# Kernel optimization log

Measured on AMD Instinct MI355X. Metric: run time of the kernel, lower is better.

The kernel has to match this reference:

```python
import jax, jax.numpy as jnp
import numpy as np

N_SITE, N_VENDOR, E = 100000, 20000, 3200000
SITE_IN, VENDOR_IN, HID, OUT = 10, 9, 64, 32


def _sage(x_src, x_dst, src, dst, n_dst, Wl, bl, Wr):
    # PyG SAGEConv (mean aggr): lin_l(mean_{e: dst(e)=i} x_src[src(e)]) + lin_r(x_dst)
    msg = x_src[src]                                   # [E, d] gather
    agg = jax.ops.segment_sum(msg, dst, num_segments=n_dst)
    cnt = jax.ops.segment_sum(jnp.ones((src.shape[0],), x_src.dtype), dst,
                              num_segments=n_dst)
    mean = agg / jnp.maximum(cnt, 1.0)[:, None]
    return mean @ Wl + bl + x_dst @ Wr


def setup_inputs() -> dict:
    key = jax.random.key(0)
    ks = jax.random.split(key, 24)
    g = lambda k, s: (jax.random.normal(k, s, jnp.float32) / np.sqrt(s[0])).astype(jnp.float32)
    inp = {
        'x_site': jax.random.normal(ks[0], (N_SITE, SITE_IN), jnp.float32),
        'x_vendor': jax.random.normal(ks[1], (N_VENDOR, VENDOR_IN), jnp.float32),
        'src': jax.random.randint(ks[2], (E,), 0, N_SITE),
        'dst': jax.random.randint(ks[3], (E,), 0, N_VENDOR),
        # input projections
        'W_site_in': g(ks[4], (SITE_IN, HID)), 'b_site_in': jnp.zeros((HID,), jnp.float32),
        'W_vendor_in': g(ks[5], (VENDOR_IN, HID)), 'b_vendor_in': jnp.zeros((HID,), jnp.float32),
        # conv1 site->vendor (64->64)
        'Wl1sv': g(ks[6], (HID, HID)), 'bl1sv': jnp.zeros((HID,), jnp.float32), 'Wr1sv': g(ks[7], (HID, HID)),
        # conv1 vendor->site (64->64)
        'Wl1vs': g(ks[8], (HID, HID)), 'bl1vs': jnp.zeros((HID,), jnp.float32), 'Wr1vs': g(ks[9], (HID, HID)),
        # conv2 site->vendor (64->32)
        'Wl2sv': g(ks[10], (HID, OUT)), 'bl2sv': jnp.zeros((OUT,), jnp.float32), 'Wr2sv': g(ks[11], (HID, OUT)),
        # conv2 vendor->site (64->32)
        'Wl2vs': g(ks[12], (HID, OUT)), 'bl2vs': jnp.zeros((OUT,), jnp.float32), 'Wr2vs': g(ks[13], (HID, OUT)),
    }
    return inp


def reference(x_site, x_vendor, src, dst,
              W_site_in, b_site_in, W_vendor_in, b_vendor_in,
              Wl1sv, bl1sv, Wr1sv, Wl1vs, bl1vs, Wr1vs,
              Wl2sv, bl2sv, Wr2sv, Wl2vs, bl2vs, Wr2vs):
    xs = x_site @ W_site_in + b_site_in        # [N_SITE, HID]
    xv = x_vendor @ W_vendor_in + b_vendor_in  # [N_VENDOR, HID]
    # layer 1 (dropout is identity in eval mode)
    xv1 = jax.nn.relu(_sage(xs, xv, src, dst, N_VENDOR, Wl1sv, bl1sv, Wr1sv))
    xs1 = jax.nn.relu(_sage(xv, xs, dst, src, N_SITE, Wl1vs, bl1vs, Wr1vs))
    # layer 2
    xv2 = jax.nn.relu(_sage(xs1, xv1, src, dst, N_VENDOR, Wl2sv, bl2sv, Wr2sv))
    xs2 = jax.nn.relu(_sage(xv1, xs1, dst, src, N_SITE, Wl2vs, bl2vs, Wr2vs))
    # concat [site; vendor] -> [N_SITE + N_VENDOR, OUT]
    return jnp.concatenate([xs2, xv2], axis=0)
```

## Files before the change

kernel.cpp:

```cpp
#include <hip/hip_runtime.h>

constexpr int N_SITE    = 100000;
constexpr int N_VENDOR  = 20000;
constexpr int NE        = 3200000;
constexpr int SITE_IN   = 10;
constexpr int VENDOR_IN = 9;
constexpr int HID       = 64;
constexpr int OUT       = 32;
constexpr int S_HALF    = 50000;

constexpr int NBLK    = 512;
constexpr int EPB     = NE / NBLK;
constexpr int SHIFT_S = 7;
constexpr int NBUK_S  = (N_SITE + 127) / 128;
constexpr int CAP_S   = 5120;
constexpr int SHIFT_V = 6;
constexpr int NBUK_V  = (N_VENDOR + 63) / 64;
constexpr int CAP_V   = 12288;

constexpr int SB1  = (N_SITE + 3) / 4;
constexpr int VB1  = (N_VENDOR + 3) / 4;
constexpr int NS_BLK = (N_SITE + 15) / 16;
constexpr int NV_BLK = (N_VENDOR + 15) / 16;
constexpr int PADTOT = 16 * (N_SITE + N_VENDOR);

constexpr long long I_NSTART_S = 0;
constexpr long long I_NDEG_S   = I_NSTART_S + N_SITE;
constexpr long long I_NSTART_V = I_NDEG_S + N_SITE;
constexpr long long I_NDEG_V   = I_NSTART_V + N_VENDOR;
constexpr long long I_NLO_V    = I_NDEG_V + N_VENDOR;
constexpr long long I_GCUR     = I_NLO_V + N_VENDOR;
constexpr long long I_ADJ_V    = (I_GCUR + NBUK_S + NBUK_V + 3) & ~3LL;
constexpr long long I_ADJ_S    = I_ADJ_V + (long long)NBUK_V * CAP_V;
constexpr long long INT_END    = (I_ADJ_S + (long long)NBUK_S * CAP_S / 2 + 3) & ~3LL;
constexpr long long A_PAIRS_S  = INT_END;
constexpr long long A_PAIRS_V  = A_PAIRS_S + (long long)NBUK_S * CAP_S;
constexpr long long BUILD_END  = A_PAIRS_V + (long long)NBUK_V * CAP_V;
constexpr long long F_Y16    = (BUILD_END + 3) & ~3LL;
constexpr long long F_PAD    = F_Y16 + (long long)(N_SITE + N_VENDOR) * 16;
constexpr long long F_FUSED  = F_PAD + (long long)(N_SITE + N_VENDOR) * 8;
constexpr long long WS_WORDS = F_FUSED + 4352;

constexpr int F_M1SV = 0;
constexpr int F_M1VS = 1024;
constexpr int F_R1SV = 2048;
constexpr int F_R1VS = 3072;
constexpr int F_V1SV = 4096;
constexpr int F_V1VS = 4160;
constexpr int F_r1SV = 4224;
constexpr int F_r1VS = 4288;

typedef _Float16 h2_t __attribute__((ext_vector_type(2)));
__device__ __forceinline__ h2_t as_h2(unsigned u) {
    union { unsigned u; h2_t h; } c; c.u = u; return c.h;
}
__device__ __forceinline__ unsigned short f2h(float f) {
    union { _Float16 h; unsigned short u; } c; c.h = (_Float16)f; return c.u;
}
#if defined(__has_builtin)
#if __has_builtin(__builtin_amdgcn_fdot2)
#define HAVE_FDOT2 1
#endif
#endif
__device__ __forceinline__ void acc2(float& slo, float& shi, unsigned u) {
#ifdef HAVE_FDOT2
    h2_t sel_lo = {(_Float16)1.0f, (_Float16)0.0f};
    h2_t sel_hi = {(_Float16)0.0f, (_Float16)1.0f};
    slo = __builtin_amdgcn_fdot2(as_h2(u), sel_lo, slo, false);
    shi = __builtin_amdgcn_fdot2(as_h2(u), sel_hi, shi, false);
#else
    h2_t h = as_h2(u);
    slo += (float)h.x; shi += (float)h.y;
#endif
}
__device__ __forceinline__ float ddot2(unsigned a, unsigned b, float c) {
#ifdef HAVE_FDOT2
    return __builtin_amdgcn_fdot2(as_h2(a), as_h2(b), c, false);
#else
    h2_t ha = as_h2(a), hb = as_h2(b);
    return c + (float)ha.x * (float)hb.x + (float)ha.y * (float)hb.y;
#endif
}

__global__ __launch_bounds__(256) void prep(
        const float* __restrict__ x_site, const float* __restrict__ x_vendor,
        unsigned short* __restrict__ xsp, unsigned short* __restrict__ xvp,
        const float* __restrict__ Wsi, const float* __restrict__ bsi,
        const float* __restrict__ Wvi, const float* __restrict__ bvi,
        const float* __restrict__ Wl1sv, const float* __restrict__ Wr1sv,
        const float* __restrict__ Wl1vs, const float* __restrict__ Wr1vs,
        float* __restrict__ fused) {
    long long t = (long long)blockIdx.x * 256 + threadIdx.x;
    if (t < (long long)N_SITE * 16) {
        int i = (int)(t >> 4), k = (int)(t & 15);
        xsp[t] = f2h(k < SITE_IN ? x_site[i * SITE_IN + k] : 0.f);
        return;
    }
    t -= (long long)N_SITE * 16;
    if (t < (long long)N_VENDOR * 16) {
        int i = (int)(t >> 4), k = (int)(t & 15);
        xvp[t] = f2h(k < VENDOR_IN ? x_vendor[i * VENDOR_IN + k] : 0.f);
        return;
    }
    t -= (long long)N_VENDOR * 16;
    int idx = (int)t;
    if (idx < 4096) {
        int m = idx >> 10, rem = idx & 1023, r = rem >> 6, c = rem & 63;
        int K = (m == 0 || m == 3) ? SITE_IN : VENDOR_IN;
        const float* A = (m == 0 || m == 3) ? Wsi : Wvi;
        const float* B = (m == 0) ? Wl1sv : (m == 1) ? Wl1vs : (m == 2) ? Wr1sv : Wr1vs;
        float s = 0.f;
        if (r < K)
            for (int j = 0; j < 64; ++j) s = fmaf(A[r * 64 + j], B[j * 64 + c], s);
        fused[idx] = s;
    } else if (idx < 4352) {
        int m = (idx - 4096) >> 6, c = idx & 63;
        const float* a = (m == 0 || m == 3) ? bsi : bvi;
        const float* B = (m == 0) ? Wl1sv : (m == 1) ? Wl1vs : (m == 2) ? Wr1sv : Wr1vs;
        float s = 0.f;
        for (int j = 0; j < 64; ++j) s = fmaf(a[j], B[j * 64 + c], s);
        fused[idx] = s;
    }
}

__global__ __launch_bounds__(256) void scatter_sort(
        const int* __restrict__ src, const int* __restrict__ dst,
        int* __restrict__ gcur,
        unsigned* __restrict__ pairs_s, unsigned* __restrict__ pairs_v) {
    __shared__ unsigned buf[EPB];
    __shared__ unsigned short bkt[EPB];
    __shared__ int hcnt[NBUK_S];
    __shared__ int loff[NBUK_S + 1];
    __shared__ int gbase[NBUK_S];
    __shared__ int sc[256];
    int blk = blockIdx.x, tid = threadIdx.x;
    int lo = blk * EPB;
    #pragma unroll 1
    for (int dir = 0; dir < 2; ++dir) {
        const int nbuk  = dir ? NBUK_V : NBUK_S;
        const int shift = dir ? SHIFT_V : SHIFT_S;
        const int* key  = dir ? dst : src;
        const int* val  = dir ? src : dst;
        const int goff  = dir ? NBUK_S : 0;
        const long long cap = dir ? CAP_V : CAP_S;
        unsigned* pairs = dir ? pairs_v : pairs_s;
        for (int i = tid; i < nbuk; i += 256) hcnt[i] = 0;
        __syncthreads();
        for (int e = lo + tid; e < lo + EPB; e += 256)
            atomicAdd(&hcnt[key[e] >> shift], 1);
        __syncthreads();
        int base_i = tid * 4;
        int c4[4], s = 0;
        #pragma unroll
        for (int k = 0; k < 4; ++k) {
            int i = base_i + k;
            int c = (i < nbuk) ? hcnt[i] : 0;
            c4[k] = s; s += c;
        }
        sc[tid] = s; __syncthreads();
        for (int st = 1; st < 256; st <<= 1) {
            int x = (tid >= st) ? sc[tid - st] : 0; __syncthreads();
            sc[tid] += x; __syncthreads();
        }
        int pre = tid ? sc[tid - 1] : 0;
        #pragma unroll
        for (int k = 0; k < 4; ++k) {
            int i = base_i + k;
            if (i < nbuk) loff[i] = pre + c4[k];
        }
        if (tid == 0) loff[nbuk] = EPB;
        __syncthreads();
        for (int i = tid; i < nbuk; i += 256) {
            int c = hcnt[i];
            gbase[i] = c ? atomicAdd(&gcur[goff + i], c) : 0;
        }
        __syncthreads();
        for (int i = tid; i < nbuk; i += 256) hcnt[i] = loff[i];
        __syncthreads();
        for (int e = lo + tid; e < lo + EPB; e += 256) {
            int kk = key[e], vv = val[e];
            int b = kk >> shift;
            int p = atomicAdd(&hcnt[b], 1);
            buf[p] = dir ? (((unsigned)(kk & 63) << 26) | (unsigned)vv)
                         : (((unsigned)(kk & 127) << 25) | (unsigned)vv);
            bkt[p] = (unsigned short)b;
        }
        __syncthreads();
        for (int t = tid; t < EPB; t += 256) {
            int b = bkt[t];
            int rel = gbase[b] + (t - loff[b]);
            if (rel < (int)cap)
                pairs[(long long)b * cap + rel] = buf[t];
        }
        __syncthreads();
    }
}

__global__ __launch_bounds__(256) void stage2both(
        const unsigned* __restrict__ pairs_s, const unsigned* __restrict__ pairs_v,
        const int* __restrict__ gcur,
        int* __restrict__ nstart_s, int* __restrict__ ndeg_s,
        int* __restrict__ nstart_v, int* __restrict__ ndeg_v,
        int* __restrict__ nlo_v,
        unsigned short* __restrict__ adj_s16, int* __restrict__ adj_v) {
    int b = blockIdx.x, tid = threadIdx.x;
    bool site = (b < NBUK_S);
    __shared__ int deg[128];
    __shared__ int cur[128];
    __shared__ int sc[256];
    if (site) {
        int lo_node = b << SHIFT_S;
        long long p0 = (long long)b * CAP_S;
        int cnt = min(gcur[b], CAP_S);
        long long p1 = p0 + cnt;
        if (tid < 128) deg[tid] = 0;
        __syncthreads();
        for (long long e = p0 + tid; e < p1; e += 256)
            atomicAdd(&deg[(int)(pairs_s[e] >> 25)], 1);
        __syncthreads();
        int d = (tid < 128) ? deg[tid] : 0;
        sc[tid] = d;
        __syncthreads();
        for (int st = 1; st < 256; st <<= 1) {
            int x = (tid >= st) ? sc[tid - st] : 0; __syncthreads();
            sc[tid] += x; __syncthreads();
        }
        int excl = sc[tid] - d;
        if (tid < 128) {
            int node = lo_node + tid;
            if (node < N_SITE) {
                nstart_s[node] = (int)(p0 + excl);
                ndeg_s[node] = d;
            }
            cur[tid] = (int)(p0 + excl);
        }
        __syncthreads();
        for (long long e = p0 + tid; e < p1; e += 256) {
            unsigned p = pairs_s[e];
            int pos = atomicAdd(&cur[(int)(p >> 25)], 1);
            adj_s16[pos] = (unsigned short)p;
        }
    } else {
        b -= NBUK_S;
        int lo_node = b << SHIFT_V;
        long long p0 = (long long)b * CAP_V;
        int cnt = min(gcur[NBUK_S + b], CAP_V);
        long long p1 = p0 + cnt;
        if (tid < 128) deg[tid] = 0;
        __syncthreads();
        for (long long e = p0 + tid; e < p1; e += 256) {
            unsigned p = pairs_v[e];
            int l = (int)(p >> 26);
            int st = (int)(p & 0x3FFFFFFu);
            atomicAdd(&deg[l], 1);
            if (st < S_HALF) atomicAdd(&deg[64 + l], 1);
        }
        __syncthreads();
        int d = (tid < 64) ? deg[tid] : 0;
        sc[tid] = d;
        __syncthreads();
        for (int st = 1; st < 256; st <<= 1) {
            int x = (tid >= st) ? sc[tid - st] : 0; __syncthreads();
            sc[tid] += x; __syncthreads();
        }
        int excl = sc[tid] - d;
        if (tid < 64) {
            int node = lo_node + tid;
            int dlo = deg[64 + tid];
            if (node < N_VENDOR) {
                nstart_v[node] = (int)(p0 + excl);
                ndeg_v[node] = d;
                nlo_v[node] = dlo;
            }
            cur[tid] = (int)(p0 + excl);
            cur[64 + tid] = (int)(p0 + excl) + dlo;
        }
        __syncthreads();
        for (long long e = p0 + tid; e < p1; e += 256) {
            unsigned p = pairs_v[e];
            int l = (int)(p >> 26);
            int st = (int)(p & 0x3FFFFFFu);
            int pos = atomicAdd((st < S_HALF) ? &cur[l] : &cur[64 + l], 1);
            adj_v[pos] = st;
        }
    }
}

template<typename IdxT>
__device__ __forceinline__ void gather1x(const unsigned short* __restrict__ fp,
                                         const IdxT* __restrict__ adj,
                                         int lo, int hi, int l16, float* s) {
    for (int j = lo + l16; j < hi; j += 16) {
        const unsigned short* row = fp + (long long)adj[j] * 16;
        uint4 q0 = *(const uint4*)row;
        unsigned u4 = *(const unsigned*)(row + 8);
        acc2(s[0], s[1], q0.x);
        acc2(s[2], s[3], q0.y);
        acc2(s[4], s[5], q0.z);
        acc2(s[6], s[7], q0.w);
        acc2(s[8], s[9], u4);
    }
}

__global__ __launch_bounds__(256) void gc1fused(
        const unsigned short* __restrict__ xsp, const unsigned short* __restrict__ xvp,
        const float* __restrict__ xs_raw, const float* __restrict__ xv_raw,
        const int* __restrict__ nstart_s, const int* __restrict__ ndeg_s,
        const unsigned short* __restrict__ adj_s16,
        const int* __restrict__ nstart_v, const int* __restrict__ ndeg_v,
        const int* __restrict__ adj_v,
        const float* __restrict__ fused,
        const float* __restrict__ bl1vs, const float* __restrict__ bl1sv,
        const float* __restrict__ Wl2sv, const float* __restrict__ Wr2vs,
        const float* __restrict__ Wl2vs, const float* __restrict__ Wr2sv,
        unsigned short* __restrict__ ys16, unsigned short* __restrict__ yv16,
        float* __restrict__ out) {
    __shared__ unsigned sWp[32 * 64];
    __shared__ unsigned sXp[16][34];
    int b = blockIdx.x, tid = threadIdx.x;
    bool site = (b < NS_BLK);
    const float *fsraw, *M, *V, *BL, *R, *RV, *Wl, *Wr;
    const int *nst, *ndg;
    unsigned short* Y; float* Z;
    int nodebase, n, kx;
    if (site) {
        nodebase = b * 16; n = N_SITE; kx = SITE_IN;
        fsraw = xs_raw; nst = nstart_s; ndg = ndeg_s;
        M = fused + F_M1VS; V = fused + F_V1VS; BL = bl1vs;
        R = fused + F_R1VS; RV = fused + F_r1VS;
        Wl = Wl2sv; Wr = Wr2vs; Y = ys16; Z = out;
    } else {
        nodebase = (b - NS_BLK) * 16; n = N_VENDOR; kx = VENDOR_IN;
        fsraw = xv_raw; nst = nstart_v; ndg = ndeg_v;
        M = fused + F_M1SV; V = fused + F_V1SV; BL = bl1sv;
        R = fused + F_R1SV; RV = fused + F_r1SV;
        Wl = Wl2vs; Wr = Wr2sv; Y = yv16;
        Z = out + (long long)N_SITE * OUT;
    }
    for (int i = tid; i < 2048; i += 256) {
        int kk = i >> 6, c = i & 63;
        int k0 = kk * 2, k1 = k0 + 1;
        float w0 = (c < 32) ? Wl[k0 * 32 + c] : Wr[k0 * 32 + (c - 32)];
        float w1 = (c < 32) ? Wl[k1 * 32 + c] : Wr[k1 * 32 + (c - 32)];
        sWp[i] = (unsigned)f2h(w0) | ((unsigned)f2h(w1) << 16);
    }
    int l16 = tid & 15, nib = tid >> 4;
    int w = nodebase + nib;
    int c0 = l16 * 4;
    if (w < n) {
        int lo = nst[w], deg = ndg[w], hi = lo + deg;
        float s[10];
        #pragma unroll
        for (int k = 0; k < 10; ++k) s[k] = 0.f;
        if (site) gather1x(xvp, adj_s16, lo, hi, l16, s);
        else      gather1x(xsp, adj_v,   lo, hi, l16, s);
        #pragma unroll
        for (int k = 0; k < 10; ++k) {
            s[k] += __shfl_xor(s[k], 1, 64);
            s[k] += __shfl_xor(s[k], 2, 64);
            s[k] += __shfl_xor(s[k], 4, 64);
            s[k] += __shfl_xor(s[k], 8, 64);
        }
        float inv = 1.0f / (float)max(deg, 1);
        float4 acc = *(const float4*)(BL + c0);
        float4 rv4 = *(const float4*)(RV + c0);
        acc.x += rv4.x; acc.y += rv4.y; acc.z += rv4.z; acc.w += rv4.w;
        if (deg > 0) {
            float4 v4 = *(const float4*)(V + c0);
            acc.x += v4.x; acc.y += v4.y; acc.z += v4.z; acc.w += v4.w;
        }
        #pragma unroll
        for (int k = 0; k < 10; ++k) {
            float m = s[k] * inv;
            float4 m4 = *(const float4*)(M + k * 64 + c0);
            acc.x = fmaf(m, m4.x, acc.x);
            acc.y = fmaf(m, m4.y, acc.y);
            acc.z = fmaf(m, m4.z, acc.z);
            acc.w = fmaf(m, m4.w, acc.w);
        }
        const float* xr = fsraw + (long long)w * kx;
        for (int k = 0; k < kx; ++k) {
            float xv = xr[k];
            float4 r4 = *(const float4*)(R + k * 64 + c0);
            acc.x = fmaf(xv, r4.x, acc.x);
            acc.y = fmaf(xv, r4.y, acc.y);
            acc.z = fmaf(xv, r4.z, acc.z);
            acc.w = fmaf(xv, r4.w, acc.w);
        }
        unsigned plo = (unsigned)f2h(fmaxf(acc.x, 0.f)) |
                       ((unsigned)f2h(fmaxf(acc.y, 0.f)) << 16);
        unsigned phi = (unsigned)f2h(fmaxf(acc.z, 0.f)) |
                       ((unsigned)f2h(fmaxf(acc.w, 0.f)) << 16);
        *(uint2*)&sXp[nib][l16 * 2] = make_uint2(plo, phi);
    }
    __syncthreads();
    int n2 = tid >> 4, q = tid & 15;
    int node = nodebase + n2;
    float4 acc = {0.f, 0.f, 0.f, 0.f};
    const unsigned* xrow = sXp[n2];
    #pragma unroll 8
    for (int kk = 0; kk < 32; ++kk) {
        unsigned xp = xrow[kk];
        uint4 wp = *(const uint4*)(sWp + kk * 64 + q * 4);
        acc.x = ddot2(xp, wp.x, acc.x);
        acc.y = ddot2(xp, wp.y, acc.y);
        acc.z = ddot2(xp, wp.z, acc.z);
        acc.w = ddot2(xp, wp.w, acc.w);
    }
    if (node < n) {
        if (q < 8) {
            unsigned p01 = (unsigned)f2h(acc.x) | ((unsigned)f2h(acc.y) << 16);
            unsigned p23 = (unsigned)f2h(acc.z) | ((unsigned)f2h(acc.w) << 16);
            *(uint2*)(Y + (long long)node * 32 + q * 4) = make_uint2(p01, p23);
        } else {
            *(float4*)(Z + (long long)node * 32 + (q - 8) * 4) = acc;
        }
    }
}

template<typename IdxT>
__device__ __forceinline__ void gather2(const unsigned short* __restrict__ y,
                                        const IdxT* __restrict__ adj,
                                        int lo, int deg, int g, int q,
                                        float& s0, float& s1, float& s2, float& s3) {
    int m = (deg > g) ? ((deg - g + 7) >> 3) : 0;
    const IdxT* ap = adj + lo + g;
    int t = 0;
    for (; t + 4 <= m; t += 4) {
        long long a0 = (long long)ap[8 * t];
        long long a1 = (long long)ap[8 * t + 8];
        long long a2 = (long long)ap[8 * t + 16];
        long long a3 = (long long)ap[8 * t + 24];
        uint2 u0 = *(const uint2*)(y + a0 * 32 + 4 * q);
        uint2 u1 = *(const uint2*)(y + a1 * 32 + 4 * q);
        uint2 u2 = *(const uint2*)(y + a2 * 32 + 4 * q);
        uint2 u3 = *(const uint2*)(y + a3 * 32 + 4 * q);
        acc2(s0, s1, u0.x); acc2(s2, s3, u0.y);
        acc2(s0, s1, u1.x); acc2(s2, s3, u1.y);
        acc2(s0, s1, u2.x); acc2(s2, s3, u2.y);
        acc2(s0, s1, u3.x); acc2(s2, s3, u3.y);
    }
    for (; t < m; ++t) {
        long long a0 = (long long)ap[8 * t];
        uint2 u0 = *(const uint2*)(y + a0 * 32 + 4 * q);
        acc2(s0, s1, u0.x); acc2(s2, s3, u0.y);
    }
}

__global__ __launch_bounds__(256) void gc2all(
        const unsigned short* __restrict__ ys16, const unsigned short* __restrict__ yv16,
        const int* __restrict__ nstart_s, const int* __restrict__ ndeg_s,
        const unsigned short* __restrict__ adj_s16,
        const int* __restrict__ nstart_v, const int* __restrict__ ndeg_v,
        const int* __restrict__ nlo_v,
        const int* __restrict__ adj_v,
        const float* __restrict__ bl2vs, const float* __restrict__ bl2sv,
        float* __restrict__ out) {
    int b = blockIdx.x;
    bool site = (b < SB1);
    const float* bias; float* o; int w, n;
    if (site) {
        w = b * 4 + (threadIdx.x >> 6); n = N_SITE;
        bias = bl2vs; o = out;
    } else {
        w = (b - SB1) * 4 + (threadIdx.x >> 6); n = N_VENDOR;
        bias = bl2sv;
        o = out + (long long)N_SITE * OUT;
    }
    if (w >= n) return;
    int lane = threadIdx.x & 63, g = lane >> 3, q = lane & 7;
    float s0 = 0.f, s1 = 0.f, s2 = 0.f, s3 = 0.f;
    int deg;
    if (site) {
        int lo = nstart_s[w]; deg = ndeg_s[w];
        gather2(yv16, adj_s16, lo, deg, g, q, s0, s1, s2, s3);
    } else {
        int lo = nstart_v[w]; deg = ndeg_v[w];
        int nlo = nlo_v[w];
        gather2(ys16, adj_v, lo, nlo, g, q, s0, s1, s2, s3);
        gather2(ys16, adj_v, lo + nlo, deg - nlo, g, q, s0, s1, s2, s3);
    }
    #pragma unroll
    for (int m = 8; m <= 32; m <<= 1) {
        s0 += __shfl_xor(s0, m, 64);
        s1 += __shfl_xor(s1, m, 64);
        s2 += __shfl_xor(s2, m, 64);
        s3 += __shfl_xor(s3, m, 64);
    }
    if (g == 0) {
        float inv = 1.0f / (float)max(deg, 1);
        float4 bz = *(const float4*)(bias + 4 * q);
        long long oi = (long long)w * 32 + 4 * q;
        float4 z = *(const float4*)(o + oi);
        float4 r;
        r.x = fmaxf(fmaf(s0, inv, bz.x + z.x), 0.f);
        r.y = fmaxf(fmaf(s1, inv, bz.y + z.y), 0.f);
        r.z = fmaxf(fmaf(s2, inv, bz.z + z.z), 0.f);
        r.w = fmaxf(fmaf(s3, inv, bz.w + z.w), 0.f);
        *(float4*)(o + oi) = r;
    }
}

extern "C" void kernel_launch(void* const* d_in, const int* in_sizes, int n_in,
                              void* d_out, int out_size, void* d_ws, size_t ws_size,
                              hipStream_t stream) {
    const float* x_site      = (const float*)d_in[0];
    const float* x_vendor    = (const float*)d_in[1];
    const int*   src         = (const int*)d_in[2];
    const int*   dst         = (const int*)d_in[3];
    const float* W_site_in   = (const float*)d_in[4];
    const float* b_site_in   = (const float*)d_in[5];
    const float* W_vendor_in = (const float*)d_in[6];
    const float* b_vendor_in = (const float*)d_in[7];
    const float* Wl1sv = (const float*)d_in[8];
    const float* bl1sv = (const float*)d_in[9];
    const float* Wr1sv = (const float*)d_in[10];
    const float* Wl1vs = (const float*)d_in[11];
    const float* bl1vs = (const float*)d_in[12];
    const float* Wr1vs = (const float*)d_in[13];
    const float* Wl2sv = (const float*)d_in[14];
    const float* bl2sv = (const float*)d_in[15];
    const float* Wr2sv = (const float*)d_in[16];
    const float* Wl2vs = (const float*)d_in[17];
    const float* bl2vs = (const float*)d_in[18];
    const float* Wr2vs = (const float*)d_in[19];

    if (ws_size < (size_t)WS_WORDS * 4) return;

    int*   wi  = (int*)d_ws;
    float* wf  = (float*)d_ws;
    float* out = (float*)d_out;

    int* nstart_s = wi + I_NSTART_S;
    int* ndeg_s   = wi + I_NDEG_S;
    int* nstart_v = wi + I_NSTART_V;
    int* ndeg_v   = wi + I_NDEG_V;
    int* nlo_v    = wi + I_NLO_V;
    int* gcur     = wi + I_GCUR;
    int* adj_v    = wi + I_ADJ_V;
    unsigned short* adj_s16 = (unsigned short*)(wi + I_ADJ_S);
    unsigned* pairs_s = (unsigned*)(wi + A_PAIRS_S);
    unsigned* pairs_v = (unsigned*)(wi + A_PAIRS_V);
    unsigned short* ys16 = (unsigned short*)(wf + F_Y16);
    unsigned short* yv16 = ys16 + (long long)N_SITE * 32;
    unsigned short* xsp  = (unsigned short*)(wf + F_PAD);
    unsigned short* xvp  = xsp + (long long)N_SITE * 16;
    float* fused = wf + F_FUSED;

    hipMemsetAsync(gcur, 0, (size_t)(NBUK_S + NBUK_V) * sizeof(int), stream);

    prep<<<(PADTOT + 4352 + 255) / 256, 256, 0, stream>>>(
        x_site, x_vendor, xsp, xvp,
        W_site_in, b_site_in, W_vendor_in, b_vendor_in,
        Wl1sv, Wr1sv, Wl1vs, Wr1vs, fused);

    scatter_sort<<<NBLK, 256, 0, stream>>>(src, dst, gcur, pairs_s, pairs_v);
    stage2both<<<NBUK_S + NBUK_V, 256, 0, stream>>>(pairs_s, pairs_v, gcur,
                                                    nstart_s, ndeg_s,
                                                    nstart_v, ndeg_v, nlo_v,
                                                    adj_s16, adj_v);

    gc1fused<<<NS_BLK + NV_BLK, 256, 0, stream>>>(
        xsp, xvp, x_site, x_vendor,
        nstart_s, ndeg_s, adj_s16, nstart_v, ndeg_v, adj_v,
        fused, bl1vs, bl1sv, Wl2sv, Wr2vs, Wl2vs, Wr2sv,
        ys16, yv16, out);

    gc2all<<<SB1 + VB1, 256, 0, stream>>>(ys16, yv16,
                                          nstart_s, ndeg_s, adj_s16,
                                          nstart_v, ndeg_v, nlo_v, adj_v,
                                          bl2vs, bl2sv, out);

    (void)in_sizes; (void)n_in; (void)out_size;
}
```

Before: 273.5 us.

## Split layer-2 gather into separate vendor-lo, vendor-hi and site kernels

```diff
diff --git a/kernel.cpp b/kernel.cpp
--- a/kernel.cpp
+++ b/kernel.cpp
@@ -39,7 +39,8 @@
 constexpr long long F_Y16    = (BUILD_END + 3) & ~3LL;
 constexpr long long F_PAD    = F_Y16 + (long long)(N_SITE + N_VENDOR) * 16;
 constexpr long long F_FUSED  = F_PAD + (long long)(N_SITE + N_VENDOR) * 8;
-constexpr long long WS_WORDS = F_FUSED + 4352;
+constexpr long long F_PART   = F_FUSED + 4352;
+constexpr long long WS_WORDS = F_PART + (long long)N_VENDOR * 32;
 
 constexpr int F_M1SV = 0;
 constexpr int F_M1VS = 1024;
@@ -447,39 +448,16 @@
     }
 }
 
-__global__ __launch_bounds__(256) void gc2all(
-        const unsigned short* __restrict__ ys16, const unsigned short* __restrict__ yv16,
-        const int* __restrict__ nstart_s, const int* __restrict__ ndeg_s,
-        const unsigned short* __restrict__ adj_s16,
-        const int* __restrict__ nstart_v, const int* __restrict__ ndeg_v,
-        const int* __restrict__ nlo_v,
-        const int* __restrict__ adj_v,
-        const float* __restrict__ bl2vs, const float* __restrict__ bl2sv,
-        float* __restrict__ out) {
-    int b = blockIdx.x;
-    bool site = (b < SB1);
-    const float* bias; float* o; int w, n;
-    if (site) {
-        w = b * 4 + (threadIdx.x >> 6); n = N_SITE;
-        bias = bl2vs; o = out;
-    } else {
-        w = (b - SB1) * 4 + (threadIdx.x >> 6); n = N_VENDOR;
-        bias = bl2sv;
-        o = out + (long long)N_SITE * OUT;
-    }
-    if (w >= n) return;
+__global__ __launch_bounds__(256) void gc2vlo(
+        const unsigned short* __restrict__ ys16,
+        const int* __restrict__ nstart_v, const int* __restrict__ nlo_v,
+        const int* __restrict__ adj_v, float* __restrict__ part) {
+    int w = blockIdx.x * 4 + (threadIdx.x >> 6);
+    if (w >= N_VENDOR) return;
     int lane = threadIdx.x & 63, g = lane >> 3, q = lane & 7;
+    int lo = nstart_v[w], nlo = nlo_v[w];
     float s0 = 0.f, s1 = 0.f, s2 = 0.f, s3 = 0.f;
-    int deg;
-    if (site) {
-        int lo = nstart_s[w]; deg = ndeg_s[w];
-        gather2(yv16, adj_s16, lo, deg, g, q, s0, s1, s2, s3);
-    } else {
-        int lo = nstart_v[w]; deg = ndeg_v[w];
-        int nlo = nlo_v[w];
-        gather2(ys16, adj_v, lo, nlo, g, q, s0, s1, s2, s3);
-        gather2(ys16, adj_v, lo + nlo, deg - nlo, g, q, s0, s1, s2, s3);
-    }
+    gather2(ys16, adj_v, lo, nlo, g, q, s0, s1, s2, s3);
     #pragma unroll
     for (int m = 8; m <= 32; m <<= 1) {
         s0 += __shfl_xor(s0, m, 64);
@@ -487,9 +465,35 @@
         s2 += __shfl_xor(s2, m, 64);
         s3 += __shfl_xor(s3, m, 64);
     }
+    if (g == 0)
+        *(float4*)(part + (long long)w * 32 + 4 * q) = make_float4(s0, s1, s2, s3);
+}
+
+__global__ __launch_bounds__(256) void gc2vhi(
+        const unsigned short* __restrict__ ys16,
+        const int* __restrict__ nstart_v, const int* __restrict__ ndeg_v,
+        const int* __restrict__ nlo_v,
+        const int* __restrict__ adj_v, const float* __restrict__ part,
+        const float* __restrict__ bl2sv, float* __restrict__ out) {
+    int w = blockIdx.x * 4 + (threadIdx.x >> 6);
+    if (w >= N_VENDOR) return;
+    int lane = threadIdx.x & 63, g = lane >> 3, q = lane & 7;
+    int lo = nstart_v[w], deg = ndeg_v[w], nlo = nlo_v[w];
+    float s0 = 0.f, s1 = 0.f, s2 = 0.f, s3 = 0.f;
+    gather2(ys16, adj_v, lo + nlo, deg - nlo, g, q, s0, s1, s2, s3);
+    #pragma unroll
+    for (int m = 8; m <= 32; m <<= 1) {
+        s0 += __shfl_xor(s0, m, 64);
+        s1 += __shfl_xor(s1, m, 64);
+        s2 += __shfl_xor(s2, m, 64);
+        s3 += __shfl_xor(s3, m, 64);
+    }
     if (g == 0) {
+        float4 p = *(const float4*)(part + (long long)w * 32 + 4 * q);
+        s0 += p.x; s1 += p.y; s2 += p.z; s3 += p.w;
         float inv = 1.0f / (float)max(deg, 1);
-        float4 bz = *(const float4*)(bias + 4 * q);
+        float4 bz = *(const float4*)(bl2sv + 4 * q);
+        float* o = out + (long long)N_SITE * OUT;
         long long oi = (long long)w * 32 + 4 * q;
         float4 z = *(const float4*)(o + oi);
         float4 r;
@@ -498,6 +502,38 @@
         r.z = fmaxf(fmaf(s2, inv, bz.z + z.z), 0.f);
         r.w = fmaxf(fmaf(s3, inv, bz.w + z.w), 0.f);
         *(float4*)(o + oi) = r;
+    }
+}
+
+__global__ __launch_bounds__(256) void gc2site(
+        const unsigned short* __restrict__ yv16,
+        const int* __restrict__ nstart_s, const int* __restrict__ ndeg_s,
+        const unsigned short* __restrict__ adj_s16,
+        const float* __restrict__ bl2vs, float* __restrict__ out) {
+    int w = blockIdx.x * 4 + (threadIdx.x >> 6);
+    if (w >= N_SITE) return;
+    int lane = threadIdx.x & 63, g = lane >> 3, q = lane & 7;
+    int lo = nstart_s[w], deg = ndeg_s[w];
+    float s0 = 0.f, s1 = 0.f, s2 = 0.f, s3 = 0.f;
+    gather2(yv16, adj_s16, lo, deg, g, q, s0, s1, s2, s3);
+    #pragma unroll
+    for (int m = 8; m <= 32; m <<= 1) {
+        s0 += __shfl_xor(s0, m, 64);
+        s1 += __shfl_xor(s1, m, 64);
+        s2 += __shfl_xor(s2, m, 64);
+        s3 += __shfl_xor(s3, m, 64);
+    }
+    if (g == 0) {
+        float inv = 1.0f / (float)max(deg, 1);
+        float4 bz = *(const float4*)(bl2vs + 4 * q);
+        long long oi = (long long)w * 32 + 4 * q;
+        float4 z = *(const float4*)(out + oi);
+        float4 r;
+        r.x = fmaxf(fmaf(s0, inv, bz.x + z.x), 0.f);
+        r.y = fmaxf(fmaf(s1, inv, bz.y + z.y), 0.f);
+        r.z = fmaxf(fmaf(s2, inv, bz.z + z.z), 0.f);
+        r.w = fmaxf(fmaf(s3, inv, bz.w + z.w), 0.f);
+        *(float4*)(out + oi) = r;
     }
 }
 
@@ -546,6 +582,7 @@
     unsigned short* xsp  = (unsigned short*)(wf + F_PAD);
     unsigned short* xvp  = xsp + (long long)N_SITE * 16;
     float* fused = wf + F_FUSED;
+    float* part  = wf + F_PART;
 
     hipMemsetAsync(gcur, 0, (size_t)(NBUK_S + NBUK_V) * sizeof(int), stream);
 
@@ -566,10 +603,10 @@
         fused, bl1vs, bl1sv, Wl2sv, Wr2vs, Wl2vs, Wr2sv,
         ys16, yv16, out);
 
-    gc2all<<<SB1 + VB1, 256, 0, stream>>>(ys16, yv16,
-                                          nstart_s, ndeg_s, adj_s16,
-                                          nstart_v, ndeg_v, nlo_v, adj_v,
-                                          bl2vs, bl2sv, out);
+    gc2vlo<<<VB1, 256, 0, stream>>>(ys16, nstart_v, nlo_v, adj_v, part);
+    gc2vhi<<<VB1, 256, 0, stream>>>(ys16, nstart_v, ndeg_v, nlo_v, adj_v, part,
+                                    bl2sv, out);
+    gc2site<<<SB1, 256, 0, stream>>>(yv16, nstart_s, ndeg_s, adj_s16, bl2vs, out);
 
     (void)in_sizes; (void)n_in; (void)out_size;
 }
```

Result: no change. 276.0 us (+0.9%).
